# Kernel tuning notes

Hardware: AMD Instinct MI355X
Metric: run time of the kernel (lower is better)

Reference implementation:

```python
import jax, jax.numpy as jnp
import numpy as np

B, IN, OUT = 2048, 64, 2048


def setup_inputs() -> dict:
    key = jax.random.key(0)
    k1, k2, k3 = jax.random.split(key, 3)
    x = jax.random.normal(k1, (B, IN), dtype=jnp.float32)
    # learned params (shapes per init: means [in, out], inv_std_dev [out, in, in])
    means = jax.random.uniform(k2, (IN, OUT), dtype=jnp.float32)
    # roughly like the inverse of a diagonal step matrix plus small noise
    inv_std_dev = (jax.random.normal(k3, (OUT, IN, IN), dtype=jnp.float32) * 0.05
                   + jnp.eye(IN, dtype=jnp.float32) * 0.5)
    return {"x": x, "means": means, "inv_std_dev": inv_std_dev}


def reference(x, means, inv_std_dev):
    # diff[b, o, i] = x[b, i] - means[i, o]   -> [B, OUT, IN]
    d = x[:, None, :] - means.T[None, :, :]
    # torch uses inv_std_dev.pow(2) (elementwise square), not a matrix square
    A = inv_std_dev * inv_std_dev  # [OUT, IN, IN]
    # per-neuron quadratic form: q[b, o] = d[b,o,:] @ A[o] @ d[b,o,:]
    q = jnp.einsum('boi,oij,boj->bo', d, A, d)
    return jnp.exp(-0.5 * q)  # [B, OUT]
```

## Files before the change

### kernel.cpp

```cpp
#include <hip/hip_runtime.h>
#include <hip/hip_bf16.h>

typedef __bf16 bf16x8 __attribute__((ext_vector_type(8)));
typedef float f32x2 __attribute__((ext_vector_type(2)));
typedef float f32x4 __attribute__((ext_vector_type(4)));
typedef float f32x16 __attribute__((ext_vector_type(16)));

#define B_N 2048
#define O_N 2048
#define K_N 64

__device__ __forceinline__ void gld16(const void* g, void* l) {
    __builtin_amdgcn_global_load_lds(
        (const __attribute__((address_space(1))) void*)g,
        (__attribute__((address_space(3))) void*)l,
        16, 0, 0);
}

__global__ __launch_bounds__(256) void rbf_prep(
    const float* __restrict__ inv, const float* __restrict__ means,
    __bf16* __restrict__ Atp, __bf16* __restrict__ cPhi,
    __bf16* __restrict__ cPlo, float* __restrict__ kArr)
{
    __shared__ float s[64 * 65];
    __shared__ float mld[64];
    __shared__ float uw[128];
    const int o = blockIdx.x;
    const int t = threadIdx.x;
    const float4* src = (const float4*)(inv + (size_t)o * 4096);
#pragma unroll
    for (int k = 0; k < 4; ++k) {
        const int idx = k * 256 + t;
        const float4 v = src[idx];
        const int i = idx >> 4;
        const int j0 = (idx & 15) * 4;
        s[i * 65 + j0 + 0] = v.x * v.x;
        s[i * 65 + j0 + 1] = v.y * v.y;
        s[i * 65 + j0 + 2] = v.z * v.z;
        s[i * 65 + j0 + 3] = v.w * v.w;
    }
    if (t < 64) mld[t] = means[(size_t)t * O_N + o];
    __syncthreads();
    if (t < 64) {
        float u = 0.f;
#pragma unroll
        for (int i = 0; i < 64; ++i) u = fmaf(s[i * 65 + t], mld[i], u);
        uw[t] = u;
    } else if (t < 128) {
        const int j = t - 64;
        float w = 0.f;
#pragma unroll
        for (int i = 0; i < 64; ++i) w = fmaf(s[j * 65 + i], mld[i], w);
        uw[64 + j] = w;
    }
    __syncthreads();
    if (t < 64) {
        const float c = -(uw[t] + uw[64 + t]);
        const __bf16 hi = (__bf16)c;
        const __bf16 lo = (__bf16)(c - (float)hi);
        const size_t eidx = (size_t)(o >> 5) * 2048 + (size_t)(t >> 4) * 512
                          + (size_t)(o & 31) * 16 + (t & 15);
        cPhi[eidx] = hi;
        cPlo[eidx] = lo;
    }
    if (t == 0) {
        float kk = 0.f;
#pragma unroll
        for (int j = 0; j < 64; ++j) kk = fmaf(uw[j], mld[j], kk);
        kArr[o] = kk;
    }
#pragma unroll
    for (int r = 0; r < 2; ++r) {
        const int ch = r * 256 + t;
        const int ss = ch >> 7;
        const int j = (ch >> 1) & 63;
        const int hh = ch & 1;
        bf16x8 v;
#pragma unroll
        for (int e = 0; e < 8; ++e)
            v[e] = (__bf16)s[(16 * ss + 8 * hh + e) * 65 + j];
        *(bf16x8*)(Atp + (size_t)o * 4096 + (size_t)ch * 8) = v;
    }
}

__global__ __launch_bounds__(256, 4) void rbf_main(
    const float* __restrict__ x, const __bf16* __restrict__ Atp,
    const __bf16* __restrict__ cPhi, const __bf16* __restrict__ cPlo,
    const float* __restrict__ kArr, float* __restrict__ out)
{
    __shared__ __align__(16) __bf16 sA[4][4096];

    const int tid = threadIdx.x;
    const int wave = tid >> 6;
    const int lane = tid & 63;
    const int b = lane & 31;
    const int h = lane >> 5;

    const int wg = (int)blockIdx.x;
    const int xcd = wg & 7;
    const int loc = wg >> 3;
    const int og = xcd * 8 + (loc >> 4);
    const int bg = loc & 15;
    const int oBase = og * 32;
    const int rowW = bg * 128 + wave * 32;

    const float* xr = x + (size_t)(rowW + b) * K_N;

    const f32x16 zz = {0.f,0.f,0.f,0.f,0.f,0.f,0.f,0.f,
                       0.f,0.f,0.f,0.f,0.f,0.f,0.f,0.f};

    bf16x8 xh[4];
    f32x4 xd[2][4];
    f32x16 lin;
    {
        bf16x8 xl[4];
#pragma unroll
        for (int ss = 0; ss < 4; ++ss) {
            const float* p = xr + ss * 16 + h * 8;
            bf16x8 vh, vl;
#pragma unroll
            for (int e = 0; e < 8; ++e) {
                const float v = p[e];
                const __bf16 hi = (__bf16)v;
                vh[e] = hi;
                vl[e] = (__bf16)(v - (float)hi);
            }
            xh[ss] = vh; xl[ss] = vl;
        }
#pragma unroll
        for (int mt = 0; mt < 2; ++mt)
#pragma unroll
            for (int rq = 0; rq < 4; ++rq)
                xd[mt][rq] = *(const f32x4*)(xr + mt * 32 + rq * 8 + h * 4);

        const __bf16* chp = cPhi + (size_t)og * 2048;
        const __bf16* clp = cPlo + (size_t)og * 2048;
        lin = zz;
#pragma unroll
        for (int ss = 0; ss < 4; ++ss) {
            const bf16x8 fh = *(const bf16x8*)(chp + ss * 512 + b * 16 + h * 8);
            const bf16x8 fl = *(const bf16x8*)(clp + ss * 512 + b * 16 + h * 8);
            lin = __builtin_amdgcn_mfma_f32_32x32x16_bf16(fh, xh[ss], lin, 0, 0, 0);
            lin = __builtin_amdgcn_mfma_f32_32x32x16_bf16(fh, xl[ss], lin, 0, 0, 0);
            lin = __builtin_amdgcn_mfma_f32_32x32x16_bf16(fl, xh[ss], lin, 0, 0, 0);
        }
#pragma unroll
        for (int r = 0; r < 16; ++r)
            lin[r] += kArr[oBase + (r & 3) + 8 * (r >> 2) + 4 * h];
    }

    const int L0 = tid * 16, L1 = 4096 + tid * 16;
    const int S0 = L0 ^ (((L0 >> 7) & 7) << 4);
    const int S1 = L1 ^ (((L1 >> 7) & 7) << 4);
    const char* gp = (const char*)(Atp + (size_t)oBase * 4096);
    gld16(gp + S0, (char*)&sA[0][0] + L0);
    gld16(gp + S1, (char*)&sA[0][0] + L1);
    gld16(gp + 8192 + S0, (char*)&sA[1][0] + L0);
    gld16(gp + 8192 + S1, (char*)&sA[1][0] + L1);

    const int off0 = (b * 32 + h * 16) ^ (((b >> 2) & 7) << 4);
    float* outp = out + (size_t)(rowW + b) * O_N + oBase;
    float q4[4];

#define RBF_COMPUTE(I) do {                                                   \
    const char* bufp_ = (const char*)&sA[(I) & 3][0];                         \
    __builtin_amdgcn_s_setprio(1);                                            \
    f32x16 a0_, a1_;                                                          \
    {                                                                         \
        const bf16x8 f0_ = *(const bf16x8*)(bufp_ + off0);                    \
        const bf16x8 f1_ = *(const bf16x8*)(bufp_ + 1024 + off0);             \
        a0_ = __builtin_amdgcn_mfma_f32_32x32x16_bf16(f0_, xh[0], zz, 0, 0, 0); \
        a1_ = __builtin_amdgcn_mfma_f32_32x32x16_bf16(f1_, xh[0], zz, 0, 0, 0); \
    }                                                                         \
    _Pragma("unroll")                                                         \
    for (int ss = 1; ss < 4; ++ss) {                                          \
        const char* base_ = bufp_ + ss * 2048;                                \
        const bf16x8 f0_ = *(const bf16x8*)(base_ + off0);                    \
        const bf16x8 f1_ = *(const bf16x8*)(base_ + 1024 + off0);             \
        a0_ = __builtin_amdgcn_mfma_f32_32x32x16_bf16(f0_, xh[ss], a0_, 0, 0, 0); \
        a1_ = __builtin_amdgcn_mfma_f32_32x32x16_bf16(f1_, xh[ss], a1_, 0, 0, 0); \
    }                                                                         \
    __builtin_amdgcn_s_setprio(0);                                            \
    f32x2 P0_ = {0.f, 0.f}, P1_ = {0.f, 0.f};                                 \
    _Pragma("unroll")                                                         \
    for (int rg = 0; rg < 4; ++rg) {                                          \
        f32x2 u_, v_;                                                         \
        u_[0] = a0_[rg*4+0]; u_[1] = a0_[rg*4+1];                             \
        v_[0] = xd[0][rg][0]; v_[1] = xd[0][rg][1];                           \
        P0_ = __builtin_elementwise_fma(u_, v_, P0_);                         \
        u_[0] = a0_[rg*4+2]; u_[1] = a0_[rg*4+3];                             \
        v_[0] = xd[0][rg][2]; v_[1] = xd[0][rg][3];                           \
        P1_ = __builtin_elementwise_fma(u_, v_, P1_);                         \
        u_[0] = a1_[rg*4+0]; u_[1] = a1_[rg*4+1];                             \
        v_[0] = xd[1][rg][0]; v_[1] = xd[1][rg][1];                           \
        P0_ = __builtin_elementwise_fma(u_, v_, P0_);                         \
        u_[0] = a1_[rg*4+2]; u_[1] = a1_[rg*4+3];                             \
        v_[0] = xd[1][rg][2]; v_[1] = xd[1][rg][3];                           \
        P1_ = __builtin_elementwise_fma(u_, v_, P1_);                         \
    }                                                                         \
    const f32x2 Ps_ = P0_ + P1_;                                              \
    float q_ = Ps_[0] + Ps_[1];                                               \
    q_ += __shfl_xor(q_, 32, 64);                                             \
    if (h == (((I) >> 2) & 1)) {                                              \
        q4[(I) & 3] = exp2f((q_ + lin[((I) & 3) + (((I) >> 3) << 2)])         \
                            * -0.72134752044448170368f);                      \
        if (((I) & 3) == 3) {                                                 \
            const f32x4 v_ = {q4[0], q4[1], q4[2], q4[3]};                    \
            *(f32x4*)(outp + ((I) - 3)) = v_;                                 \
        }                                                                     \
    }                                                                         \
} while (0)

#define RBF_PHASE(P) do {                                                     \
    __syncthreads();                                                          \
    if ((P) < 15) {                                                           \
        const char* g2_ = gp + (size_t)(2 * (P) + 2) * 8192;                  \
        char* d2_ = (char*)&sA[(2 * (P) + 2) & 3][0];                         \
        gld16(g2_ + S0, d2_ + L0);                                            \
        gld16(g2_ + S1, d2_ + L1);                                            \
        const char* g3_ = gp + (size_t)(2 * (P) + 3) * 8192;                  \
        char* d3_ = (char*)&sA[(2 * (P) + 3) & 3][0];                         \
        gld16(g3_ + S0, d3_ + L0);                                            \
        gld16(g3_ + S1, d3_ + L1);                                            \
    }                                                                         \
    RBF_COMPUTE(2 * (P));                                                     \
    RBF_COMPUTE(2 * (P) + 1);                                                 \
} while (0)

    RBF_PHASE(0);  RBF_PHASE(1);  RBF_PHASE(2);  RBF_PHASE(3);
    RBF_PHASE(4);  RBF_PHASE(5);  RBF_PHASE(6);  RBF_PHASE(7);
    RBF_PHASE(8);  RBF_PHASE(9);  RBF_PHASE(10); RBF_PHASE(11);
    RBF_PHASE(12); RBF_PHASE(13); RBF_PHASE(14); RBF_PHASE(15);

#undef RBF_PHASE
#undef RBF_COMPUTE
}

extern "C" void kernel_launch(void* const* d_in, const int* in_sizes, int n_in,
                              void* d_out, int out_size, void* d_ws, size_t ws_size,
                              hipStream_t stream)
{
    const float* x = (const float*)d_in[0];
    const float* means = (const float*)d_in[1];
    const float* inv = (const float*)d_in[2];
    float* out = (float*)d_out;

    char* w = (char*)d_ws;
    __bf16* Atp  = (__bf16*)w;
    __bf16* cPhi = (__bf16*)(w + (size_t)O_N * 4096 * 2);
    __bf16* cPlo = (__bf16*)(w + (size_t)O_N * 4096 * 2 + 262144);
    float*  kArr = (float*)(w + (size_t)O_N * 4096 * 2 + 524288);

    rbf_prep<<<dim3(O_N), dim3(256), 0, stream>>>(inv, means, Atp, cPhi, cPlo, kArr);
    rbf_main<<<dim3(1024), dim3(256), 0, stream>>>(x, Atp, cPhi, cPlo, kArr, out);

    (void)in_sizes; (void)n_in; (void)out_size; (void)ws_size;
}
```

Before: 60.65 us.

## Software-pipeline MFMA and epilogue dot across consecutive output chunks

Restructures the main loop so the VALU dot-product/exp epilogue for chunk I-1 runs while the MFMAs for chunk I are issued. All LDS fragment reads for a chunk are hoisted ahead of its MFMAs. The epilogue is also changed to add the linear term before the cross-half shuffle and to compute exp on both halves, which drops a branch around the shuffle. This costs extra accumulator registers (two more f32x16), which can raise register pressure at launch bounds of 4 waves per SIMD.

```diff
diff --git a/kernel.cpp b/kernel.cpp
--- a/kernel.cpp
+++ b/kernel.cpp
@@ -91,7 +91,6 @@
     __shared__ __align__(16) __bf16 sA[4][4096];
 
     const int tid = threadIdx.x;
-    const int wave = tid >> 6;
     const int lane = tid & 63;
     const int b = lane & 31;
     const int h = lane >> 5;
@@ -102,7 +101,7 @@
     const int og = xcd * 8 + (loc >> 4);
     const int bg = loc & 15;
     const int oBase = og * 32;
-    const int rowW = bg * 128 + wave * 32;
+    const int rowW = bg * 128 + (tid >> 6) * 32;
 
     const float* xr = x + (size_t)(rowW + b) * K_N;
 
@@ -161,57 +160,59 @@
     const int off0 = (b * 32 + h * 16) ^ (((b >> 2) & 7) << 4);
     float* outp = out + (size_t)(rowW + b) * O_N + oBase;
     float q4[4];
-
-#define RBF_COMPUTE(I) do {                                                   \
-    const char* bufp_ = (const char*)&sA[(I) & 3][0];                         \
-    __builtin_amdgcn_s_setprio(1);                                            \
-    f32x16 a0_, a1_;                                                          \
-    {                                                                         \
-        const bf16x8 f0_ = *(const bf16x8*)(bufp_ + off0);                    \
-        const bf16x8 f1_ = *(const bf16x8*)(bufp_ + 1024 + off0);             \
-        a0_ = __builtin_amdgcn_mfma_f32_32x32x16_bf16(f0_, xh[0], zz, 0, 0, 0); \
-        a1_ = __builtin_amdgcn_mfma_f32_32x32x16_bf16(f1_, xh[0], zz, 0, 0, 0); \
-    }                                                                         \
-    _Pragma("unroll")                                                         \
-    for (int ss = 1; ss < 4; ++ss) {                                          \
-        const char* base_ = bufp_ + ss * 2048;                                \
-        const bf16x8 f0_ = *(const bf16x8*)(base_ + off0);                    \
-        const bf16x8 f1_ = *(const bf16x8*)(base_ + 1024 + off0);             \
-        a0_ = __builtin_amdgcn_mfma_f32_32x32x16_bf16(f0_, xh[ss], a0_, 0, 0, 0); \
-        a1_ = __builtin_amdgcn_mfma_f32_32x32x16_bf16(f1_, xh[ss], a1_, 0, 0, 0); \
-    }                                                                         \
-    __builtin_amdgcn_s_setprio(0);                                            \
+    f32x16 a0, a1, aP0, aP1;
+
+#define RBF_DOT(A0, A1, I) do {                                               \
     f32x2 P0_ = {0.f, 0.f}, P1_ = {0.f, 0.f};                                 \
     _Pragma("unroll")                                                         \
     for (int rg = 0; rg < 4; ++rg) {                                          \
         f32x2 u_, v_;                                                         \
-        u_[0] = a0_[rg*4+0]; u_[1] = a0_[rg*4+1];                             \
+        u_[0] = (A0)[rg*4+0]; u_[1] = (A0)[rg*4+1];                           \
         v_[0] = xd[0][rg][0]; v_[1] = xd[0][rg][1];                           \
         P0_ = __builtin_elementwise_fma(u_, v_, P0_);                         \
-        u_[0] = a0_[rg*4+2]; u_[1] = a0_[rg*4+3];                             \
+        u_[0] = (A0)[rg*4+2]; u_[1] = (A0)[rg*4+3];                           \
         v_[0] = xd[0][rg][2]; v_[1] = xd[0][rg][3];                           \
         P1_ = __builtin_elementwise_fma(u_, v_, P1_);                         \
-        u_[0] = a1_[rg*4+0]; u_[1] = a1_[rg*4+1];                             \
+        u_[0] = (A1)[rg*4+0]; u_[1] = (A1)[rg*4+1];                           \
         v_[0] = xd[1][rg][0]; v_[1] = xd[1][rg][1];                           \
         P0_ = __builtin_elementwise_fma(u_, v_, P0_);                         \
-        u_[0] = a1_[rg*4+2]; u_[1] = a1_[rg*4+3];                             \
+        u_[0] = (A1)[rg*4+2]; u_[1] = (A1)[rg*4+3];                           \
         v_[0] = xd[1][rg][2]; v_[1] = xd[1][rg][3];                           \
         P1_ = __builtin_elementwise_fma(u_, v_, P1_);                         \
     }                                                                         \
     const f32x2 Ps_ = P0_ + P1_;                                              \
-    float q_ = Ps_[0] + Ps_[1];                                               \
-    q_ += __shfl_xor(q_, 32, 64);                                             \
-    if (h == (((I) >> 2) & 1)) {                                              \
-        q4[(I) & 3] = exp2f((q_ + lin[((I) & 3) + (((I) >> 3) << 2)])         \
-                            * -0.72134752044448170368f);                      \
-        if (((I) & 3) == 3) {                                                 \
-            const f32x4 v_ = {q4[0], q4[1], q4[2], q4[3]};                    \
-            *(f32x4*)(outp + ((I) - 3)) = v_;                                 \
-        }                                                                     \
-    }                                                                         \
-} while (0)
-
-#define RBF_PHASE(P) do {                                                     \
+    float qh_ = Ps_[0] + Ps_[1];                                              \
+        \
+    qh_ += (h == (((I) >> 2) & 1)) ? lin[((I) & 3) + (((I) >> 3) << 2)] : 0.f;\
+    const float q_ = qh_ + __shfl_xor(qh_, 32, 64);                           \
+    q4[(I) & 3] = exp2f(q_ * -0.72134752044448170368f);                       \
+    if (((I) & 3) == 3 && h == (((I) >> 2) & 1)) {                            \
+        const f32x4 v_ = {q4[0], q4[1], q4[2], q4[3]};                        \
+        *(f32x4*)(outp + ((I) - 3)) = v_;                                     \
+    }                                                                         \
+} while (0)
+
+#define RBF_READS(G, BUF) do {                                                \
+    _Pragma("unroll")                                                         \
+    for (int ss = 0; ss < 4; ++ss) {                                          \
+        (G)[2*ss]   = *(const bf16x8*)((BUF) + ss * 2048 + off0);             \
+        (G)[2*ss+1] = *(const bf16x8*)((BUF) + ss * 2048 + 1024 + off0);      \
+    }                                                                         \
+} while (0)
+
+#define RBF_MFMA(G, A0, A1) do {                                              \
+    __builtin_amdgcn_s_setprio(1);                                            \
+    (A0) = __builtin_amdgcn_mfma_f32_32x32x16_bf16((G)[0], xh[0], zz, 0, 0, 0); \
+    (A1) = __builtin_amdgcn_mfma_f32_32x32x16_bf16((G)[1], xh[0], zz, 0, 0, 0); \
+    _Pragma("unroll")                                                         \
+    for (int ss = 1; ss < 4; ++ss) {                                          \
+        (A0) = __builtin_amdgcn_mfma_f32_32x32x16_bf16((G)[2*ss],   xh[ss], (A0), 0, 0, 0); \
+        (A1) = __builtin_amdgcn_mfma_f32_32x32x16_bf16((G)[2*ss+1], xh[ss], (A1), 0, 0, 0); \
+    }                                                                         \
+    __builtin_amdgcn_s_setprio(0);                                            \
+} while (0)
+
+#define RBF_PAIR(P) do {                                                      \
     __syncthreads();                                                          \
     if ((P) < 15) {                                                           \
         const char* g2_ = gp + (size_t)(2 * (P) + 2) * 8192;                  \
@@ -223,17 +224,29 @@
         gld16(g3_ + S0, d3_ + L0);                                            \
         gld16(g3_ + S1, d3_ + L1);                                            \
     }                                                                         \
-    RBF_COMPUTE(2 * (P));                                                     \
-    RBF_COMPUTE(2 * (P) + 1);                                                 \
-} while (0)
-
-    RBF_PHASE(0);  RBF_PHASE(1);  RBF_PHASE(2);  RBF_PHASE(3);
-    RBF_PHASE(4);  RBF_PHASE(5);  RBF_PHASE(6);  RBF_PHASE(7);
-    RBF_PHASE(8);  RBF_PHASE(9);  RBF_PHASE(10); RBF_PHASE(11);
-    RBF_PHASE(12); RBF_PHASE(13); RBF_PHASE(14); RBF_PHASE(15);
-
-#undef RBF_PHASE
-#undef RBF_COMPUTE
+    const char* b0_ = (const char*)&sA[(2 * (P)) & 3][0];                     \
+    bf16x8 g0_[8];                                                            \
+    RBF_READS(g0_, b0_);                                                      \
+    if ((P) > 0) RBF_DOT(aP0, aP1, 2 * (P) - 1);                              \
+    RBF_MFMA(g0_, a0, a1);                                                    \
+    const char* b1_ = (const char*)&sA[(2 * (P) + 1) & 3][0];                 \
+    bf16x8 g1_[8];                                                            \
+    RBF_READS(g1_, b1_);                                                      \
+    RBF_DOT(a0, a1, 2 * (P));                                                 \
+    RBF_MFMA(g1_, aP0, aP1);                                                  \
+} while (0)
+
+    RBF_PAIR(0);  RBF_PAIR(1);  RBF_PAIR(2);  RBF_PAIR(3);
+    RBF_PAIR(4);  RBF_PAIR(5);  RBF_PAIR(6);  RBF_PAIR(7);
+    RBF_PAIR(8);  RBF_PAIR(9);  RBF_PAIR(10); RBF_PAIR(11);
+    RBF_PAIR(12); RBF_PAIR(13); RBF_PAIR(14); RBF_PAIR(15);
+
+    RBF_DOT(aP0, aP1, 31);
+
+#undef RBF_PAIR
+#undef RBF_MFMA
+#undef RBF_READS
+#undef RBF_DOT
 }
 
 extern "C" void kernel_launch(void* const* d_in, const int* in_sizes, int n_in,
```

New measurement: 84.54 us. +39.4%, slower.
